# Kernel tuning notes

Hardware: AMD Instinct MI355X
Metric: run time of the kernel (lower is better)

Reference implementation:

```python
import jax, jax.numpy as jnp
import numpy as np

M_DIM = 1024
H_DIM = 1024
NEG = -1e9


def setup_inputs() -> dict:
    key = jax.random.key(0)
    ks = jax.random.split(key, 9)
    B, S = 4, 2048
    q = jax.random.normal(ks[0], (B, S, M_DIM), dtype=jnp.float32)
    k = jax.random.normal(ks[1], (B, S, M_DIM), dtype=jnp.float32)
    v = jax.random.normal(ks[2], (B, S, M_DIM), dtype=jnp.float32)
    attention_mask = jnp.ones((B, S), dtype=jnp.int32)
    sc = 1.0 / np.sqrt(M_DIM)
    Wq_w = jax.random.normal(ks[3], (H_DIM, M_DIM), dtype=jnp.float32) * sc
    Wq_b = jnp.zeros((H_DIM,), dtype=jnp.float32)
    Wk_w = jax.random.normal(ks[4], (H_DIM, M_DIM), dtype=jnp.float32) * sc
    Wk_b = jnp.zeros((H_DIM,), dtype=jnp.float32)
    Wv_w = jax.random.normal(ks[5], (H_DIM, M_DIM), dtype=jnp.float32) * sc
    Wv_b = jnp.zeros((H_DIM,), dtype=jnp.float32)
    return {"q": q, "k": k, "v": v, "attention_mask": attention_mask,
            "Wq_w": Wq_w, "Wq_b": Wq_b, "Wk_w": Wk_w, "Wk_b": Wk_b,
            "Wv_w": Wv_w, "Wv_b": Wv_b}


def reference(q, k, v, attention_mask, Wq_w, Wq_b, Wk_w, Wk_b, Wv_w, Wv_b):
    # Linear projections (torch Linear: x @ W.T + b)
    qh = jnp.einsum('bsm,hm->bsh', q, Wq_w) + Wq_b
    kh = jnp.einsum('bsm,hm->bsh', k, Wk_w) + Wk_b
    vh = jnp.einsum('bsm,hm->bsh', v, Wv_w) + Wv_b
    # Scaled dot-product scores: [B, Sq, Sk]
    scores = jnp.einsum('bqh,bkh->bqk', qh, kh) / jnp.sqrt(jnp.float32(H_DIM))
    # Padding mask: attention_mask [B, Sk] -> [B, 1, Sk]
    pad = attention_mask.astype(bool)[:, None, :]
    scores = jnp.where(pad, scores, NEG)
    # Causal mask (apply_mask=True)
    Sq, Sk = scores.shape[1], scores.shape[2]
    causal = jnp.tril(jnp.ones((Sq, Sk), dtype=bool))
    scores = jnp.where(causal[None, :, :], scores, NEG)
    attn = jax.nn.softmax(scores, axis=-1)
    out = jnp.einsum('bqk,bkh->bqh', attn, vh)
    # dropout is identity in eval mode
    return out
```

## Files before the change

### kernel.cpp

```cpp
#include <hip/hip_runtime.h>
#include <stdint.h>


typedef __attribute__((ext_vector_type(8))) short s8v;
typedef __attribute__((ext_vector_type(4))) float f4v;

__device__ __forceinline__ unsigned short f2bf(float f) {
    union { float f; unsigned u; } v; v.f = f;
    unsigned u = v.u;
    u = u + 0x7fffu + ((u >> 16) & 1u);
    return (unsigned short)(u >> 16);
}

__device__ __forceinline__ void gld_lds16(const void* gptr, void* lptr) {
    __builtin_amdgcn_global_load_lds(
        (const __attribute__((address_space(1))) unsigned int*)(uintptr_t)gptr,
        (__attribute__((address_space(3))) unsigned int*)(unsigned int)(uintptr_t)lptr,
        16, 0, 0);
}

__global__ __launch_bounds__(256) void convert_all(
    const float* __restrict__ q, const float* __restrict__ k, const float* __restrict__ v,
    const float* __restrict__ wq, const float* __restrict__ wk, const float* __restrict__ wv,
    unsigned short* __restrict__ qb, unsigned short* __restrict__ kb, unsigned short* __restrict__ vb,
    unsigned short* __restrict__ wqb, unsigned short* __restrict__ wkb, unsigned short* __restrict__ wvb,
    float* __restrict__ l)
{
    int b = blockIdx.x;
    if (b >= 27648) {
        int li = (b - 27648) * 256 + threadIdx.x;
        l[li] = 0.f;
        return;
    }
    const float* src; unsigned short* dst; int blk;
    if (b < 8192)       { src = q;  dst = qb;  blk = b; }
    else if (b < 16384) { src = k;  dst = kb;  blk = b - 8192; }
    else if (b < 24576) { src = v;  dst = vb;  blk = b - 16384; }
    else if (b < 25600) { src = wq; dst = wqb; blk = b - 24576; }
    else if (b < 26624) { src = wk; dst = wkb; blk = b - 25600; }
    else                { src = wv; dst = wvb; blk = b - 26624; }
    size_t idx = (size_t)blk * 1024 + (size_t)threadIdx.x * 4;
    float4 f = *(const float4*)(src + idx);
    ushort4 o = make_ushort4(f2bf(f.x), f2bf(f.y), f2bf(f.z), f2bf(f.w));
    *(ushort4*)(dst + idx) = o;
}

__device__ __forceinline__ void gemm_tiles(
    const unsigned short* __restrict__ A, int lda,
    const unsigned short* __restrict__ Bt, int ldb,
    int m0, int n0, int kTiles,
    unsigned short* As, unsigned short* Bs,
    f4v acc[4][4])
{
    const int t    = threadIdx.x;
    const int lane = t & 63;
    const int wave = t >> 6;
    const int wm   = (wave >> 1) * 64;
    const int wn   = (wave & 1) * 64;
    const int l15  = lane & 15;
    const int quad = lane >> 4;

    const int c0 = t, c1 = t + 256;
    unsigned short* As0 = As + (c0 & ~63) * 8;
    unsigned short* As1 = As + (c1 & ~63) * 8;
    unsigned short* Bs0 = Bs + (c0 & ~63) * 8;
    unsigned short* Bs1 = Bs + (c1 & ~63) * 8;
    const unsigned short* Ag0 = A  + (size_t)(m0 + (c0 >> 2)) * lda + (c0 & 3) * 8;
    const unsigned short* Ag1 = A  + (size_t)(m0 + (c1 >> 2)) * lda + (c1 & 3) * 8;
    const unsigned short* Bg0 = Bt + (size_t)(n0 + (c0 >> 2)) * ldb + (c0 & 3) * 8;
    const unsigned short* Bg1 = Bt + (size_t)(n0 + (c1 >> 2)) * ldb + (c1 & 3) * 8;

    const unsigned short* a_base = As + quad * 8;
    const unsigned short* b_base = Bs + quad * 8;

    gld_lds16(Ag0, As0);
    gld_lds16(Ag1, As1);
    gld_lds16(Bg0, Bs0);
    gld_lds16(Bg1, Bs1);

    for (int kt = 0; kt < kTiles; ++kt) {
        __syncthreads();
        Ag0 += 32; Ag1 += 32; Bg0 += 32; Bg1 += 32;
        if (kt + 1 < kTiles) {
            const int nb = ((kt + 1) & 1) * 4096;
            gld_lds16(Ag0, As0 + nb);
            gld_lds16(Ag1, As1 + nb);
            gld_lds16(Bg0, Bs0 + nb);
            gld_lds16(Bg1, Bs1 + nb);
        }
        const int cb = (kt & 1) * 4096;
        s8v af[4], bf[4];
        #pragma unroll
        for (int i = 0; i < 4; ++i)
            af[i] = *(const s8v*)(a_base + cb + (wm + i * 16 + l15) * 32);
        #pragma unroll
        for (int j = 0; j < 4; ++j)
            bf[j] = *(const s8v*)(b_base + cb + (wn + j * 16 + l15) * 32);
        #pragma unroll
        for (int i = 0; i < 4; ++i)
            #pragma unroll
            for (int j = 0; j < 4; ++j)
                acc[i][j] = __builtin_amdgcn_mfma_f32_16x16x32_bf16(af[i], bf[j], acc[i][j], 0, 0, 0);
    }
}

#define ACC_INIT  f4v acc[4][4]; { f4v z = {0.f,0.f,0.f,0.f}; \
    _Pragma("unroll") for (int i = 0; i < 4; ++i) \
    _Pragma("unroll") for (int j = 0; j < 4; ++j) acc[i][j] = z; }

#define LANE_VARS \
    const int lane = threadIdx.x & 63; const int wave = threadIdx.x >> 6; \
    const int wm = (wave >> 1) * 64;  const int wn = (wave & 1) * 64; \
    const int l15 = lane & 15;        const int quad = lane >> 4;

__global__ __launch_bounds__(512, 2) void proj_qk(
    const unsigned short* __restrict__ qb, const unsigned short* __restrict__ wqb,
    const float* __restrict__ bq, unsigned short* __restrict__ QH,
    const unsigned short* __restrict__ kb, const unsigned short* __restrict__ wkb,
    const float* __restrict__ bk, unsigned short* __restrict__ KH)
{
    const int z = blockIdx.z;
    const unsigned short* X; const unsigned short* W; const float* bias; unsigned short* Y;
    if (z == 0) { X = qb; W = wqb; bias = bq; Y = QH; }
    else        { X = kb; W = wkb; bias = bk; Y = KH; }

    __shared__ __align__(16) unsigned short As[2 * 256 * 64];
    __shared__ __align__(16) unsigned short Bs[2 * 256 * 64];

    const int t    = threadIdx.x;
    const int lane = t & 63;
    const int w    = t >> 6;
    const int wm   = (w >> 2) * 128;
    const int wn   = (w & 3) * 64;
    const int l15  = lane & 15;
    const int quad = lane >> 4;
    const int m0   = blockIdx.x * 256;
    const int n0   = blockIdx.y * 256;
    enum { KT = 16 };

    const int r0 = t >> 3;
    const int sw = (t & 7) ^ (r0 & 7);
    const unsigned short* gA = X + (size_t)(m0 + r0) * 1024 + sw * 8;
    const unsigned short* gB = W + (size_t)(n0 + r0) * 1024 + sw * 8;
    unsigned short* lA = As + (t & ~63) * 8;
    unsigned short* lB = Bs + (t & ~63) * 8;

#define PSTAGE_A(b, h, kt) { \
    gld_lds16(gA + (size_t)(h) * 131072 + (kt) * 64,         lA + (b) * 16384 + (h) * 8192); \
    gld_lds16(gA + (size_t)(h) * 131072 + 65536 + (kt) * 64, lA + (b) * 16384 + (h) * 8192 + 4096); }
#define PSTAGE_B(b, h, kt) { \
    gld_lds16(gB + (size_t)(h) * 131072 + (kt) * 64,         lB + (b) * 16384 + (h) * 8192); \
    gld_lds16(gB + (size_t)(h) * 131072 + 65536 + (kt) * 64, lB + (b) * 16384 + (h) * 8192 + 4096); }

    const int aoff = (wm + l15) * 64;
    const int boff = (wn + l15) * 64;
    const int seg0 = ((quad    ) ^ (l15 & 7)) * 8;
    const int seg1 = ((quad | 4) ^ (l15 & 7)) * 8;

    f4v acc[8][4];
    { f4v zz = {0.f, 0.f, 0.f, 0.f};
      #pragma unroll
      for (int i = 0; i < 8; ++i)
        #pragma unroll
        for (int j = 0; j < 4; ++j) acc[i][j] = zz; }
    s8v a[8], b0[4], b1[4];

    PSTAGE_A(0, 0, 0); PSTAGE_A(0, 1, 0); PSTAGE_B(0, 0, 0); PSTAGE_B(0, 1, 0);
    PSTAGE_B(1, 0, 1); PSTAGE_A(1, 0, 1);
    asm volatile("s_waitcnt vmcnt(4)" ::: "memory");
    __builtin_amdgcn_s_barrier();

    for (int kt = 0; kt < KT; ++kt) {
        const int p  = kt & 1;
        const int np = p ^ 1;
        const unsigned short* Ar = As + p * 16384 + aoff;
        const unsigned short* Br = Bs + p * 16384 + boff;

        #pragma unroll
        for (int i = 0; i < 4; ++i) {
            a[i * 2]     = *(const s8v*)(Ar + i * 1024 + seg0);
            a[i * 2 + 1] = *(const s8v*)(Ar + i * 1024 + seg1);
        }
        #pragma unroll
        for (int j = 0; j < 2; ++j) {
            b0[j * 2]     = *(const s8v*)(Br + j * 1024 + seg0);
            b0[j * 2 + 1] = *(const s8v*)(Br + j * 1024 + seg1);
        }
        #pragma unroll
        for (int j = 0; j < 2; ++j) {
            b1[j * 2]     = *(const s8v*)(Br + 2048 + j * 1024 + seg0);
            b1[j * 2 + 1] = *(const s8v*)(Br + 2048 + j * 1024 + seg1);
        }
        if (kt + 1 < KT) PSTAGE_A(np, 1, kt + 1);
        __builtin_amdgcn_s_setprio(1);
        #pragma unroll
        for (int i = 0; i < 4; ++i)
            #pragma unroll
            for (int j = 0; j < 2; ++j) {
                acc[i][j] = __builtin_amdgcn_mfma_f32_16x16x32_bf16(a[i*2],   b0[j*2],   acc[i][j], 0, 0, 0);
                acc[i][j] = __builtin_amdgcn_mfma_f32_16x16x32_bf16(a[i*2+1], b0[j*2+1], acc[i][j], 0, 0, 0);
            }
        __builtin_amdgcn_s_setprio(0);
        if (kt + 1 < KT) PSTAGE_B(np, 1, kt + 1);
        __builtin_amdgcn_s_setprio(1);
        #pragma unroll
        for (int i = 0; i < 4; ++i)
            #pragma unroll
            for (int j = 0; j < 2; ++j) {
                acc[i][2+j] = __builtin_amdgcn_mfma_f32_16x16x32_bf16(a[i*2],   b1[j*2],   acc[i][2+j], 0, 0, 0);
                acc[i][2+j] = __builtin_amdgcn_mfma_f32_16x16x32_bf16(a[i*2+1], b1[j*2+1], acc[i][2+j], 0, 0, 0);
            }
        __builtin_amdgcn_s_setprio(0);
        #pragma unroll
        for (int i = 0; i < 4; ++i) {
            a[i * 2]     = *(const s8v*)(Ar + 4096 + i * 1024 + seg0);
            a[i * 2 + 1] = *(const s8v*)(Ar + 4096 + i * 1024 + seg1);
        }
        __builtin_amdgcn_s_barrier();
        if (kt + 2 < KT) PSTAGE_B(p, 0, kt + 2);
        __builtin_amdgcn_s_setprio(1);
        #pragma unroll
        for (int i = 0; i < 4; ++i)
            #pragma unroll
            for (int j = 0; j < 2; ++j) {
                acc[4+i][2+j] = __builtin_amdgcn_mfma_f32_16x16x32_bf16(a[i*2],   b1[j*2],   acc[4+i][2+j], 0, 0, 0);
                acc[4+i][2+j] = __builtin_amdgcn_mfma_f32_16x16x32_bf16(a[i*2+1], b1[j*2+1], acc[4+i][2+j], 0, 0, 0);
            }
        __builtin_amdgcn_s_setprio(0);
        __builtin_amdgcn_s_barrier();
        if (kt + 2 < KT) PSTAGE_A(p, 0, kt + 2);
        __builtin_amdgcn_s_setprio(1);
        #pragma unroll
        for (int i = 0; i < 4; ++i)
            #pragma unroll
            for (int j = 0; j < 2; ++j) {
                acc[4+i][j] = __builtin_amdgcn_mfma_f32_16x16x32_bf16(a[i*2],   b0[j*2],   acc[4+i][j], 0, 0, 0);
                acc[4+i][j] = __builtin_amdgcn_mfma_f32_16x16x32_bf16(a[i*2+1], b0[j*2+1], acc[4+i][j], 0, 0, 0);
            }
        __builtin_amdgcn_s_setprio(0);
        if (kt + 2 < KT) { asm volatile("s_waitcnt vmcnt(4)" ::: "memory"); }
        else             { asm volatile("s_waitcnt vmcnt(0)" ::: "memory"); }
        __builtin_amdgcn_s_barrier();
    }
#undef PSTAGE_A
#undef PSTAGE_B

    #pragma unroll
    for (int ig = 0; ig < 8; ++ig) {
        int row = m0 + wm + ig * 16 + quad * 4;
        #pragma unroll
        for (int jg = 0; jg < 4; ++jg) {
            int col = n0 + wn + jg * 16 + l15;
            float bvv = bias[col];
            #pragma unroll
            for (int r = 0; r < 4; ++r)
                Y[(size_t)(row + r) * 1024 + col] = f2bf(acc[ig][jg][r] + bvv);
        }
    }
}

__global__ __launch_bounds__(256) void proj_v(
    const unsigned short* __restrict__ vb, const unsigned short* __restrict__ wvb,
    const float* __restrict__ bv, unsigned short* __restrict__ VHT)
{
    __shared__ __align__(16) unsigned short As[2 * 128 * 32];
    __shared__ __align__(16) unsigned short Bs[2 * 128 * 32];
    const int m0 = blockIdx.x * 128;
    const int n0 = blockIdx.y * 128;
    ACC_INIT;
    gemm_tiles(vb, 1024, wvb, 1024, m0, n0, 32, As, Bs, acc);
    LANE_VARS;
    #pragma unroll
    for (int i = 0; i < 4; ++i) {
        int row = m0 + wm + i * 16 + quad * 4;
        int bb = row >> 11;
        int s  = row & 2047;
        #pragma unroll
        for (int j = 0; j < 4; ++j) {
            int col = n0 + wn + j * 16 + l15;
            float bvv = bv[col];
            ushort4 o = make_ushort4(f2bf(acc[i][j][0] + bvv), f2bf(acc[i][j][1] + bvv),
                                     f2bf(acc[i][j][2] + bvv), f2bf(acc[i][j][3] + bvv));
            *(ushort4*)(VHT + (size_t)bb * (1024 * 2048) + (size_t)col * 2048 + s) = o;
        }
    }
}

__global__ __launch_bounds__(256) void score_kernel(
    const unsigned short* __restrict__ QH, const unsigned short* __restrict__ KH,
    const int* __restrict__ mask, unsigned short* __restrict__ P, float* __restrict__ lsum)
{
    const int b = blockIdx.y;
    int tq = blockIdx.x;
    int qt = 0;
    while ((qt + 1) * (qt + 2) / 2 <= tq) ++qt;
    const int kt = tq - qt * (qt + 1) / 2;

    __shared__ __align__(16) unsigned short As[2 * 128 * 32];
    __shared__ __align__(16) unsigned short Bs[2 * 128 * 32];
    const unsigned short* A  = QH + (size_t)b * 2048 * 1024;
    const unsigned short* Bt = KH + (size_t)b * 2048 * 1024;
    unsigned short* Pb = P + (size_t)b * 2048 * 2048;
    float* lb = lsum + b * 2048;
    const int* mb = mask + b * 2048;
    const int m0 = qt * 128, n0 = kt * 128;
    ACC_INIT;
    gemm_tiles(A, 1024, Bt, 1024, m0, n0, 32, As, Bs, acc);
    LANE_VARS;
    float rs[4][4];
    #pragma unroll
    for (int i = 0; i < 4; ++i)
        #pragma unroll
        for (int r = 0; r < 4; ++r) rs[i][r] = 0.f;
    #pragma unroll
    for (int i = 0; i < 4; ++i) {
        int qbase = m0 + wm + i * 16 + quad * 4;
        #pragma unroll
        for (int j = 0; j < 4; ++j) {
            int kg = n0 + wn + j * 16 + l15;
            int mv = mb[kg];
            #pragma unroll
            for (int r = 0; r < 4; ++r) {
                float s = acc[i][j][r] * 0.03125f;
                float p = (mv && (kg <= qbase + r)) ? __expf(s) : 0.f;
                Pb[(size_t)(qbase + r) * 2048 + kg] = f2bf(p);
                rs[i][r] += p;
            }
        }
    }
    #pragma unroll
    for (int i = 0; i < 4; ++i)
        #pragma unroll
        for (int r = 0; r < 4; ++r) {
            float v_ = rs[i][r];
            v_ += __shfl_xor(v_, 1);
            v_ += __shfl_xor(v_, 2);
            v_ += __shfl_xor(v_, 4);
            v_ += __shfl_xor(v_, 8);
            if (l15 == 0)
                atomicAdd(&lb[m0 + wm + i * 16 + quad * 4 + r], v_);
        }
}

__constant__ int pv_qt[24] = {15,15, 7,14,14,13,13, 6,12,12,11,11, 5,10,10, 9, 9, 4, 8, 8, 3, 2, 1, 0};
__constant__ int pv_ks[24] = { 0,32, 0, 0,30, 0,28, 0, 0,26, 0,24, 0, 0,22, 0,20, 0, 0,18, 0, 0, 0, 0};
__constant__ int pv_kc[24] = {32,32,32,30,30,28,28,28,26,26,24,24,24,22,22,20,20,20,18,18,16,12, 8, 4};

__global__ __launch_bounds__(256) void pv_kernel(
    const unsigned short* __restrict__ P, const unsigned short* __restrict__ VHT,
    const float* __restrict__ lsum, float* __restrict__ Out, float* __restrict__ Part)
{
    const int nt = blockIdx.x, y = blockIdx.y, b = blockIdx.z;
    const int qt = pv_qt[y], kstart = pv_ks[y], kcount = pv_kc[y];

    __shared__ __align__(16) unsigned short As[2 * 128 * 32];
    __shared__ __align__(16) unsigned short Bs[2 * 128 * 32];
    const unsigned short* A  = P   + (size_t)b * 2048 * 2048 + (size_t)kstart * 32;
    const unsigned short* Bt = VHT + (size_t)b * 1024 * 2048 + (size_t)kstart * 32;
    const float* lb = lsum + b * 2048;
    const int m0 = qt * 128, n0 = nt * 128;
    ACC_INIT;
    gemm_tiles(A, 2048, Bt, 2048, m0, n0, kcount, As, Bs, acc);
    LANE_VARS;
    float* dst; int rowoff;
    if (kstart == 0) { dst = Out  + (size_t)b * 2048 * 1024; rowoff = 0; }
    else             { dst = Part + (size_t)b * 1024 * 1024; rowoff = -1024; }
    #pragma unroll
    for (int i = 0; i < 4; ++i) {
        int q0 = m0 + wm + i * 16 + quad * 4;
        float inv[4];
        #pragma unroll
        for (int r = 0; r < 4; ++r) inv[r] = 1.0f / lb[q0 + r];
        #pragma unroll
        for (int j = 0; j < 4; ++j) {
            int h = n0 + wn + j * 16 + l15;
            #pragma unroll
            for (int r = 0; r < 4; ++r)
                dst[(size_t)(q0 + r + rowoff) * 1024 + h] = acc[i][j][r] * inv[r];
        }
    }
}

__global__ __launch_bounds__(256) void add_partial(
    float4* __restrict__ Out4, const float4* __restrict__ Part4)
{
    int i = blockIdx.x * 256 + threadIdx.x;
    int b = i >> 18;
    int rem = i & 262143;
    int oi = b * 524288 + 262144 + rem;
    float4 o = Out4[oi], p = Part4[i];
    o.x += p.x; o.y += p.y; o.z += p.z; o.w += p.w;
    Out4[oi] = o;
}

extern "C" void kernel_launch(void* const* d_in, const int* in_sizes, int n_in,
                              void* d_out, int out_size, void* d_ws, size_t ws_size,
                              hipStream_t stream)
{
    const float* q    = (const float*)d_in[0];
    const float* k    = (const float*)d_in[1];
    const float* v    = (const float*)d_in[2];
    const int*   mask = (const int*)d_in[3];
    const float* Wq   = (const float*)d_in[4];
    const float* bq   = (const float*)d_in[5];
    const float* Wk   = (const float*)d_in[6];
    const float* bk   = (const float*)d_in[7];
    const float* Wv   = (const float*)d_in[8];
    const float* bv   = (const float*)d_in[9];
    float* out = (float*)d_out;

    char* ws = (char*)d_ws;
    size_t off = 0;
    auto take = [&](size_t bytes) { char* p = ws + off; off += (bytes + 255) & ~(size_t)255; return p; };
    unsigned short* qb  = (unsigned short*)take(8192ull * 1024 * 2);
    unsigned short* kb  = (unsigned short*)take(8192ull * 1024 * 2);
    unsigned short* vb  = (unsigned short*)take(8192ull * 1024 * 2);
    unsigned short* wqb = (unsigned short*)take(1024ull * 1024 * 2);
    unsigned short* wkb = (unsigned short*)take(1024ull * 1024 * 2);
    unsigned short* wvb = (unsigned short*)take(1024ull * 1024 * 2);
    unsigned short* QH  = (unsigned short*)take(8192ull * 1024 * 2);
    unsigned short* KH  = (unsigned short*)take(8192ull * 1024 * 2);
    unsigned short* VHT = (unsigned short*)take(8192ull * 1024 * 2);
    unsigned short* P   = (unsigned short*)take(4ull * 2048 * 2048 * 2);
    float*          l   = (float*)take(4ull * 2048 * 4);
    float*          Part = (float*)qb;

    convert_all<<<27680, 256, 0, stream>>>(q, k, v, Wq, Wk, Wv,
                                           qb, kb, vb, wqb, wkb, wvb, l);
    proj_qk<<<dim3(32, 4, 2), 512, 0, stream>>>(qb, wqb, bq, QH,
                                                kb, wkb, bk, KH);
    proj_v<<<dim3(64, 8), 256, 0, stream>>>(vb, wvb, bv, VHT);
    score_kernel<<<dim3(136, 4), 256, 0, stream>>>(QH, KH, mask, P, l);
    pv_kernel<<<dim3(8, 24, 4), 256, 0, stream>>>(P, VHT, l, out, Part);
    add_partial<<<4096, 256, 0, stream>>>((float4*)out, (const float4*)Part);
}
```

Baseline: 301.6 us.

## Remap block indices for XCD-aware L2 reuse and widen conversion loads

The projection, score and PV kernels move to 1D grids whose block index is remapped so that blocks sharing the same A-tile (all N tiles for a given M tile) are consecutive in launch order. Consecutive blocks land on different XCDs, so the intent appears to be better L2/MALL reuse of shared operands across the chiplets. Separately, the fp32-to-bf16 conversion kernel now handles 8 elements per thread with 16-byte stores and half as many blocks, cutting launch and instruction overhead. The score kernel spreads triangle tiles with a stride-17 permutation, which may change load balance as well as locality.

```diff
diff --git a/kernel.cpp b/kernel.cpp
--- a/kernel.cpp
+++ b/kernel.cpp
@@ -27,22 +27,29 @@
     float* __restrict__ l)
 {
     int b = blockIdx.x;
-    if (b >= 27648) {
-        int li = (b - 27648) * 256 + threadIdx.x;
-        l[li] = 0.f;
+    if (b >= 13824) {
+        int li = (b - 13824) * 2048 + threadIdx.x * 8;
+        float4 z = {0.f, 0.f, 0.f, 0.f};
+        *(float4*)(l + li) = z;
+        *(float4*)(l + li + 4) = z;
         return;
     }
     const float* src; unsigned short* dst; int blk;
-    if (b < 8192)       { src = q;  dst = qb;  blk = b; }
-    else if (b < 16384) { src = k;  dst = kb;  blk = b - 8192; }
-    else if (b < 24576) { src = v;  dst = vb;  blk = b - 16384; }
-    else if (b < 25600) { src = wq; dst = wqb; blk = b - 24576; }
-    else if (b < 26624) { src = wk; dst = wkb; blk = b - 25600; }
-    else                { src = wv; dst = wvb; blk = b - 26624; }
-    size_t idx = (size_t)blk * 1024 + (size_t)threadIdx.x * 4;
-    float4 f = *(const float4*)(src + idx);
-    ushort4 o = make_ushort4(f2bf(f.x), f2bf(f.y), f2bf(f.z), f2bf(f.w));
-    *(ushort4*)(dst + idx) = o;
+    if (b < 4096)       { src = q;  dst = qb;  blk = b; }
+    else if (b < 8192)  { src = k;  dst = kb;  blk = b - 4096; }
+    else if (b < 12288) { src = v;  dst = vb;  blk = b - 8192; }
+    else if (b < 12800) { src = wq; dst = wqb; blk = b - 12288; }
+    else if (b < 13312) { src = wk; dst = wkb; blk = b - 12800; }
+    else                { src = wv; dst = wvb; blk = b - 13312; }
+    size_t idx = (size_t)blk * 2048 + (size_t)threadIdx.x * 8;
+    float4 f0 = *(const float4*)(src + idx);
+    float4 f1 = *(const float4*)(src + idx + 4);
+    s8v o;
+    o[0] = (short)f2bf(f0.x); o[1] = (short)f2bf(f0.y);
+    o[2] = (short)f2bf(f0.z); o[3] = (short)f2bf(f0.w);
+    o[4] = (short)f2bf(f1.x); o[5] = (short)f2bf(f1.y);
+    o[6] = (short)f2bf(f1.z); o[7] = (short)f2bf(f1.w);
+    *(s8v*)(dst + idx) = o;
 }
 
 __device__ __forceinline__ void gemm_tiles(
@@ -119,7 +126,11 @@
     const unsigned short* __restrict__ kb, const unsigned short* __restrict__ wkb,
     const float* __restrict__ bk, unsigned short* __restrict__ KH)
 {
-    const int z = blockIdx.z;
+    const int w_ = blockIdx.x;
+    const int yz = w_ & 7;
+    const int ny = yz & 3;
+    const int z  = yz >> 2;
+    const int mx = w_ >> 3;
     const unsigned short* X; const unsigned short* W; const float* bias; unsigned short* Y;
     if (z == 0) { X = qb; W = wqb; bias = bq; Y = QH; }
     else        { X = kb; W = wkb; bias = bk; Y = KH; }
@@ -134,8 +145,8 @@
     const int wn   = (w & 3) * 64;
     const int l15  = lane & 15;
     const int quad = lane >> 4;
-    const int m0   = blockIdx.x * 256;
-    const int n0   = blockIdx.y * 256;
+    const int m0   = mx * 256;
+    const int n0   = ny * 256;
     enum { KT = 16 };
 
     const int r0 = t >> 3;
@@ -265,8 +276,9 @@
 {
     __shared__ __align__(16) unsigned short As[2 * 128 * 32];
     __shared__ __align__(16) unsigned short Bs[2 * 128 * 32];
-    const int m0 = blockIdx.x * 128;
-    const int n0 = blockIdx.y * 128;
+    const int w_ = blockIdx.x;
+    const int m0 = (w_ >> 3) * 128;
+    const int n0 = (w_ & 7) * 128;
     ACC_INIT;
     gemm_tiles(vb, 1024, wvb, 1024, m0, n0, 32, As, Bs, acc);
     LANE_VARS;
@@ -291,7 +303,8 @@
     const int* __restrict__ mask, unsigned short* __restrict__ P, float* __restrict__ lsum)
 {
     const int b = blockIdx.y;
-    int tq = blockIdx.x;
+    const int bx = blockIdx.x;
+    int tq = (bx & 7) * 17 + (bx >> 3);
     int qt = 0;
     while ((qt + 1) * (qt + 2) / 2 <= tq) ++qt;
     const int kt = tq - qt * (qt + 1) / 2;
@@ -350,7 +363,11 @@
     const unsigned short* __restrict__ P, const unsigned short* __restrict__ VHT,
     const float* __restrict__ lsum, float* __restrict__ Out, float* __restrict__ Part)
 {
-    const int nt = blockIdx.x, y = blockIdx.y, b = blockIdx.z;
+    const int w_  = blockIdx.x;
+    const int nt  = w_ & 7;
+    const int idx = w_ >> 3;
+    const int b   = idx / 24;
+    const int y   = idx % 24;
     const int qt = pv_qt[y], kstart = pv_ks[y], kcount = pv_kc[y];
 
     __shared__ __align__(16) unsigned short As[2 * 128 * 32];
@@ -425,12 +442,12 @@
     float*          l   = (float*)take(4ull * 2048 * 4);
     float*          Part = (float*)qb;
 
-    convert_all<<<27680, 256, 0, stream>>>(q, k, v, Wq, Wk, Wv,
+    convert_all<<<13828, 256, 0, stream>>>(q, k, v, Wq, Wk, Wv,
                                            qb, kb, vb, wqb, wkb, wvb, l);
-    proj_qk<<<dim3(32, 4, 2), 512, 0, stream>>>(qb, wqb, bq, QH,
-                                                kb, wkb, bk, KH);
-    proj_v<<<dim3(64, 8), 256, 0, stream>>>(vb, wvb, bv, VHT);
+    proj_qk<<<256, 512, 0, stream>>>(qb, wqb, bq, QH,
+                                     kb, wkb, bk, KH);
+    proj_v<<<512, 256, 0, stream>>>(vb, wvb, bv, VHT);
     score_kernel<<<dim3(136, 4), 256, 0, stream>>>(QH, KH, mask, P, l);
-    pv_kernel<<<dim3(8, 24, 4), 256, 0, stream>>>(P, VHT, l, out, Part);
+    pv_kernel<<<768, 256, 0, stream>>>(P, VHT, l, out, Part);
     add_partial<<<4096, 256, 0, stream>>>((float4*)out, (const float4*)Part);
 }
```

New measurement: 300.8 us. No clear change (-0.3%).
